# Kernel optimization log

Measured on AMD Instinct MI355X. Metric: run time of the kernel, lower is better.

Reference implementation:

```python
import jax, jax.numpy as jnp
import numpy as np

N, E, D, SD, SH, EA, FC, H = 50000, 800000, 128, 64, 16, 32, 128, 8
EPS = 1e-5


def setup_inputs() -> dict:
    key = jax.random.key(0)
    ks = jax.random.split(key, 20)
    rn = lambda k, shp, fan: jax.random.normal(k, shp, jnp.float32) / np.sqrt(fan).astype(np.float32)
    return {
        'node_features': jax.random.normal(ks[0], (N, D), jnp.float32),
        'edge_attr': jax.random.normal(ks[1], (E, EA), jnp.float32),
        'edge_sh': jax.random.normal(ks[2], (E, SH), jnp.float32),
        'W_node': rn(ks[3], (D, D), D),
        'fc1': rn(ks[4], (EA, FC), EA), 'b1': jnp.zeros((FC,), jnp.float32),
        'fc2': rn(ks[5], (FC, FC), FC), 'b2': jnp.zeros((FC,), jnp.float32),
        'fc3': rn(ks[6], (FC, D), FC), 'b3': jnp.zeros((D,), jnp.float32),
        'W_sh': rn(ks[7], (SH, D), SH),
        'aW1': rn(ks[8], (2 * SD + EA, FC), 2 * SD + EA), 'ab1': jnp.zeros((FC,), jnp.float32),
        'aW2': rn(ks[9], (FC, FC), FC), 'ab2': jnp.zeros((FC,), jnp.float32),
        'aW3': rn(ks[10], (FC, H), FC), 'ab3': jnp.zeros((H,), jnp.float32),
        'W_out': rn(ks[11], (D, D), D),
        'edge_index': jax.random.randint(ks[12], (2, E), 0, N, jnp.int32),
        'batch': jnp.zeros((N,), jnp.int32),
    }


def reference(node_features, edge_attr, edge_sh, W_node, fc1, b1, fc2, b2, fc3, b3,
              W_sh, aW1, ab1, aW2, ab2, aW3, ab3, W_out, edge_index, batch):
    src, dst = edge_index[0], edge_index[1]
    x_src = node_features[src]                          # [E, D] gather
    # SeparableFCTP message MLP: radial FC net gates a depthwise TP with edge_sh
    h = jax.nn.silu(edge_attr @ fc1 + b1)
    h = jax.nn.silu(h @ fc2 + b2)
    scale = h @ fc3 + b3                                # [E, D] per-channel radial weights
    msg = jax.nn.silu((x_src @ W_node) * scale + edge_sh @ W_sh)  # [E, D]
    # edge attention over scalar channels (softmax over the edge dim, as in source)
    alpha_in = jnp.concatenate([x_src[:, :SD], node_features[dst, :SD], edge_attr], axis=-1)
    a = jax.nn.silu(alpha_in @ aW1 + ab1)
    a = jax.nn.silu(a @ aW2 + ab2)
    a = a @ aW3 + ab3                                   # [E, H]
    alpha = jax.nn.softmax(a, axis=0)
    alpha_mean = alpha.mean(axis=1, keepdims=True)      # [E, 1]
    agg = jax.ops.segment_sum(msg * alpha_mean, dst, num_segments=node_features.shape[0])
    out = node_features + agg @ W_out                   # dropout is identity in eval
    mu = out.mean(axis=-1, keepdims=True)
    var = out.var(axis=-1, keepdims=True)
    return (out - mu) / jnp.sqrt(var + EPS)
```

## Files before the change

kernel.cpp:

```cpp
#include <hip/hip_runtime.h>
#include <math.h>

#define N_NODES 50000
#define N_EDGES 800000
#define DIM     128
#define SDIM    64
#define SH_DIM  16
#define EA_DIM  32
#define FC_DIM  128
#define H_HEADS 8
#define AIN_DIM 160
#define LN_EPS  1e-5f

typedef __attribute__((ext_vector_type(8))) short short8;
typedef __attribute__((ext_vector_type(4))) short short4v;
typedef __attribute__((ext_vector_type(4))) float f32x4;

#define FR_FC1 0
#define FR_FC2 512
#define FR_FC3 2560
#define FR_WND 4608
#define FR_WSH 6656
#define FR_AW1 7168
#define FR_AW2 9728
#define FR_AW3 11776
#define FR_TOTAL 12032

__device__ __forceinline__ float silu(float x) {
    return x * __builtin_amdgcn_rcpf(1.0f + __expf(-x));
}

__device__ __forceinline__ unsigned short f2bf(float x) {
    unsigned u = __float_as_uint(x);
    return (unsigned short)((u + 0x7FFFu + ((u >> 16) & 1u)) >> 16);
}
__device__ __forceinline__ float bf2f(unsigned short h) { return __uint_as_float(((unsigned)h) << 16); }

__device__ __forceinline__ unsigned int fmap(float f) {
    unsigned int b = __float_as_uint(f);
    return (b & 0x80000000u) ? ~b : (b | 0x80000000u);
}
__device__ __forceinline__ float funmap(unsigned int u) {
    return (u & 0x80000000u) ? __uint_as_float(u & 0x7FFFFFFFu) : __uint_as_float(~u);
}

template<int KSTEPS, int NT, int STRIDE>
__device__ __forceinline__ void mm_acc(const char* aBase, int rowBase, int lane,
                                       const short8* __restrict__ bfrag, f32x4* acc)
{
    const int row  = rowBase + (lane & 15);
    const int swz  = (row & 7) << 4;
    const int rb   = row * STRIDE;
    const int koff = (lane >> 4) << 4;
    #pragma unroll
    for (int ks = 0; ks < KSTEPS; ++ks) {
        short8 a = *(const short8*)(aBase + ((rb + ks * 64 + koff) ^ swz));
        #pragma unroll
        for (int ct = 0; ct < NT; ++ct) {
            short8 b = bfrag[(ks * NT + ct) * 64 + lane];
            acc[ct] = __builtin_amdgcn_mfma_f32_16x16x32_bf16(a, b, acc[ct], 0, 0, 0);
        }
    }
}

template<int STRIDE>
__device__ __forceinline__ void store_rows_silu(char* base, int rowBase, int lane,
                                                const f32x4* acc, const float* __restrict__ bias)
{
    const int l15  = lane & 15;
    const int col2 = l15 * 2;
    #pragma unroll
    for (int ct = 0; ct < 8; ++ct) {
        const float bv = bias[ct * 16 + l15];
        #pragma unroll
        for (int r = 0; r < 4; ++r) {
            const int row = rowBase + ((lane >> 4) * 4) + r;
            const float v = silu(acc[ct][r] + bv);
            const int off = (row * STRIDE + ct * 32 + col2) ^ ((row & 7) << 4);
            *(short*)(base + off) = (short)f2bf(v);
        }
    }
}

__device__ __forceinline__ void zero8(f32x4* a) {
    #pragma unroll
    for (int i = 0; i < 8; ++i) a[i] = (f32x4){0.f, 0.f, 0.f, 0.f};
}

__global__ void k_prep(const float* __restrict__ fc1, const float* __restrict__ fc2,
                       const float* __restrict__ fc3, const float* __restrict__ W_node,
                       const float* __restrict__ W_sh, const float* __restrict__ aW1,
                       const float* __restrict__ aW2, const float* __restrict__ aW3,
                       short8* __restrict__ frags)
{
    const int gid = blockIdx.x * 256 + threadIdx.x;
    const float* src; int Ksrc, Nsrc, Nld, NT, base;
    if (gid < 2560) {
        if (gid < 512)  { src = fc1;  Ksrc = 32;  Nsrc = 128; Nld = 128; NT = 8; base = FR_FC1; }
        else            { src = fc2;  Ksrc = 128; Nsrc = 128; Nld = 128; NT = 8; base = FR_FC2; }
    } else if (gid < 6656) {
        if (gid < 4608) { src = fc3;    Ksrc = 128; Nsrc = 128; Nld = 128; NT = 8; base = FR_FC3; }
        else            { src = W_node; Ksrc = 128; Nsrc = 128; Nld = 128; NT = 8; base = FR_WND; }
    } else if (gid < 9728) {
        if (gid < 7168) { src = W_sh; Ksrc = 16;  Nsrc = 128; Nld = 128; NT = 8; base = FR_WSH; }
        else            { src = aW1;  Ksrc = 160; Nsrc = 128; Nld = 128; NT = 8; base = FR_AW1; }
    } else {
        if (gid < 11776){ src = aW2;  Ksrc = 128; Nsrc = 128; Nld = 128; NT = 8; base = FR_AW2; }
        else            { src = aW3;  Ksrc = 128; Nsrc = 8;   Nld = 8;   NT = 1; base = FR_AW3; }
    }
    const int local = gid - base;
    const int lane = local & 63;
    const int tmp  = local >> 6;
    const int ct   = tmp % NT;
    const int ks   = tmp / NT;
    const int col  = ct * 16 + (lane & 15);
    const int k0   = ks * 32 + ((lane >> 4) << 3);
    unsigned short o[8];
    #pragma unroll
    for (int i = 0; i < 8; ++i) {
        const int k = k0 + i;
        const float v = (k < Ksrc && col < Nsrc) ? src[(size_t)k * Nld + col] : 0.f;
        o[i] = f2bf(v);
    }
    unsigned a = (unsigned)o[0] | ((unsigned)o[1] << 16);
    unsigned b = (unsigned)o[2] | ((unsigned)o[3] << 16);
    unsigned c = (unsigned)o[4] | ((unsigned)o[5] << 16);
    unsigned d = (unsigned)o[6] | ((unsigned)o[7] << 16);
    ((uint4*)frags)[gid] = make_uint4(a, b, c, d);
}

__global__ void k0_init(float* __restrict__ aggz, unsigned int* __restrict__ cmax,
                        float* __restrict__ csum)
{
    const int total = N_NODES * (DIM / 2);
    for (int i = blockIdx.x * blockDim.x + threadIdx.x; i < total;
         i += gridDim.x * blockDim.x)
        aggz[i] = 0.0f;
    if (blockIdx.x == 0 && threadIdx.x < H_HEADS) {
        cmax[threadIdx.x] = fmap(-3.0e38f);
        csum[threadIdx.x] = 0.0f;
    }
}

__global__ __launch_bounds__(256, 2) void k1_logits(
    const float* __restrict__ nodef, const float* __restrict__ eattr,
    const float* __restrict__ ab1, const float* __restrict__ ab2,
    const float* __restrict__ ab3,
    const short8* __restrict__ frags,
    const int* __restrict__ srcp, const int* __restrict__ dstp,
    float* __restrict__ a_out, unsigned int* __restrict__ cmax)
{
    __shared__ __align__(16) char sBuf[64 * 512 + 64 * 256];
    char* sAIN = sBuf;
    char* sG1  = sBuf + 64 * 512;
    char* sG2  = sBuf;
    __shared__ int sid[64], did[64];
    __shared__ float wmaxL[32];

    const int tid = threadIdx.x;
    const int e0  = blockIdx.x * 64;

    if (tid < 64)            sid[tid]      = srcp[e0 + tid];
    else if (tid < 128)      did[tid - 64] = dstp[e0 + tid - 64];
    __syncthreads();

    for (int idx = tid; idx < 64 * 40; idx += 256) {
        const int e = idx / 40, q = idx - e * 40;
        float4 v; int k;
        if (q < 16)      { v = ((const float4*)(nodef + (size_t)sid[e] * DIM))[q];      k = q * 4; }
        else if (q < 32) { v = ((const float4*)(nodef + (size_t)did[e] * DIM))[q - 16]; k = 64 + (q - 16) * 4; }
        else             { v = ((const float4*)(eattr + (size_t)(e0 + e) * EA_DIM))[q - 32]; k = 128 + (q - 32) * 4; }
        short4v h = {(short)f2bf(v.x), (short)f2bf(v.y), (short)f2bf(v.z), (short)f2bf(v.w)};
        *(short4v*)(sAIN + ((e * 512 + k * 2) ^ ((e & 7) << 4))) = h;
    }
    __syncthreads();

    const int lane = tid & 63, w = tid >> 6;
    const int rowBase = w * 16;
    f32x4 g[8];

    zero8(g);
    mm_acc<5, 8, 512>(sAIN, rowBase, lane, frags + FR_AW1, g);
    store_rows_silu<256>(sG1, rowBase, lane, g, ab1);
    __syncthreads();

    zero8(g);
    mm_acc<4, 8, 256>(sG1, rowBase, lane, frags + FR_AW2, g);
    store_rows_silu<256>(sG2, rowBase, lane, g, ab2);
    __syncthreads();

    f32x4 p = {0.f, 0.f, 0.f, 0.f};
    mm_acc<4, 1, 256>(sG2, rowBase, lane, frags + FR_AW3, &p);

    const int h = lane & 15;
    float vmax = -3.0e38f;
    if (h < H_HEADS) {
        const float ab = ab3[h];
        #pragma unroll
        for (int r = 0; r < 4; ++r) {
            const int row = rowBase + ((lane >> 4) * 4) + r;
            const float v = p[r] + ab;
            a_out[(size_t)(e0 + row) * H_HEADS + h] = v;
            vmax = fmaxf(vmax, v);
        }
    }
    vmax = fmaxf(vmax, __shfl_xor(vmax, 16));
    vmax = fmaxf(vmax, __shfl_xor(vmax, 32));
    if (lane < 8) wmaxL[w * 8 + lane] = vmax;
    __syncthreads();
    if (tid < 8) {
        const float m = fmaxf(fmaxf(wmaxL[tid], wmaxL[8 + tid]),
                              fmaxf(wmaxL[16 + tid], wmaxL[24 + tid]));
        atomicMax(&cmax[tid], fmap(m));
    }
}

__global__ void k2_expsum(const float* __restrict__ a_buf,
                          const unsigned int* __restrict__ cmax,
                          float* __restrict__ csum)
{
    __shared__ float partial[4][8];
    const int tid = threadIdx.x;
    const int h   = tid & 7;
    const float M = funmap(cmax[h]);
    float s = 0.f;
    const int total = N_EDGES * H_HEADS;
    const int stride = gridDim.x * 256;
    for (int i = blockIdx.x * 256 + tid; i < total; i += stride)
        s += __expf(a_buf[i] - M);
    s += __shfl_xor(s, 8);
    s += __shfl_xor(s, 16);
    s += __shfl_xor(s, 32);
    const int wave = tid >> 6, lane = tid & 63;
    if (lane < 8) partial[wave][lane] = s;
    __syncthreads();
    if (tid < 8) {
        float t = partial[0][tid] + partial[1][tid] + partial[2][tid] + partial[3][tid];
        atomicAdd(&csum[tid], t);
    }
}

__global__ __launch_bounds__(256, 2) void k3_message(
    const float* __restrict__ nodef, const float* __restrict__ eattr,
    const float* __restrict__ esh,
    const float* __restrict__ b1, const float* __restrict__ b2,
    const float* __restrict__ b3,
    const short8* __restrict__ frags,
    const int* __restrict__ srcp, const int* __restrict__ dstp,
    const float* __restrict__ a_buf, const unsigned int* __restrict__ cmax,
    const float* __restrict__ csum,
    unsigned short* __restrict__ aggB)
{
    __shared__ __align__(16) char sBuf[49152];
    char* sXS = sBuf;
    char* sEA = sBuf + 16384;
    char* sSH = sBuf + 24576;
    char* sH1 = sBuf + 32768;
    char* sH2 = sBuf + 16384;
    __shared__ float amL[64];
    __shared__ int sidL[64], didL[64];

    const int tid = threadIdx.x;
    const int e0  = blockIdx.x * 64;

    if (tid < 64)       sidL[tid]      = srcp[e0 + tid];
    else if (tid < 128) didL[tid - 64] = dstp[e0 + tid - 64];
    __syncthreads();

    for (int idx = tid; idx < 64 * 32; idx += 256) {
        const int e = idx >> 5, q = idx & 31;
        float4 v = ((const float4*)(nodef + (size_t)sidL[e] * DIM))[q];
        short4v h = {(short)f2bf(v.x), (short)f2bf(v.y), (short)f2bf(v.z), (short)f2bf(v.w)};
        *(short4v*)(sXS + ((e * 256 + q * 8) ^ ((e & 7) << 4))) = h;
    }
    for (int idx = tid; idx < 64 * 8; idx += 256) {
        const int e = idx >> 3, q = idx & 7;
        float4 v = ((const float4*)(eattr + (size_t)(e0 + e) * EA_DIM))[q];
        short4v h = {(short)f2bf(v.x), (short)f2bf(v.y), (short)f2bf(v.z), (short)f2bf(v.w)};
        *(short4v*)(sEA + ((e * 128 + q * 8) ^ ((e & 7) << 4))) = h;
    }
    for (int idx = tid; idx < 64 * 8; idx += 256) {
        const int e = idx >> 3, q = idx & 7;
        short4v h = {0, 0, 0, 0};
        if (q < 4) {
            float4 v = ((const float4*)(esh + (size_t)(e0 + e) * SH_DIM))[q];
            h = (short4v){(short)f2bf(v.x), (short)f2bf(v.y), (short)f2bf(v.z), (short)f2bf(v.w)};
        }
        *(short4v*)(sSH + ((e * 128 + q * 8) ^ ((e & 7) << 4))) = h;
    }
    if (tid < 64) {
        float s = 0.f;
        #pragma unroll
        for (int h = 0; h < H_HEADS; ++h)
            s += __expf(a_buf[(size_t)(e0 + tid) * H_HEADS + h] - funmap(cmax[h])) / csum[h];
        amL[tid] = s * (1.0f / H_HEADS);
    }
    __syncthreads();

    const int lane = tid & 63, w = tid >> 6;
    const int rowBase = w * 16;
    const int l15 = lane & 15;
    f32x4 sc[8], xw[8], sw[8];

    zero8(sw);
    mm_acc<1, 8, 128>(sSH, rowBase, lane, frags + FR_WSH, sw);

    zero8(sc);
    mm_acc<1, 8, 128>(sEA, rowBase, lane, frags + FR_FC1, sc);
    store_rows_silu<256>(sH1, rowBase, lane, sc, b1);
    __syncthreads();

    zero8(sc);
    mm_acc<4, 8, 256>(sH1, rowBase, lane, frags + FR_FC2, sc);
    store_rows_silu<256>(sH2, rowBase, lane, sc, b2);
    __syncthreads();

    zero8(sc);
    mm_acc<4, 8, 256>(sH2, rowBase, lane, frags + FR_FC3, sc);
    #pragma unroll
    for (int ct = 0; ct < 8; ++ct) sc[ct] += b3[ct * 16 + l15];

    zero8(xw);
    mm_acc<4, 8, 256>(sXS, rowBase, lane, frags + FR_WND, xw);

    #pragma unroll
    for (int r = 0; r < 4; ++r) {
        const int row = rowBase + ((lane >> 4) * 4) + r;
        const float am = amL[row];
        const unsigned long long abase =
            (unsigned long long)(aggB) + (unsigned long long)didL[row] * (DIM * 2);
        #pragma unroll
        for (int cp = 0; cp < 4; ++cp) {
            const float m0 = silu(xw[2*cp][r]   * sc[2*cp][r]   + sw[2*cp][r])   * am;
            const float m1 = silu(xw[2*cp+1][r] * sc[2*cp+1][r] + sw[2*cp+1][r]) * am;
            const unsigned u  = (unsigned)f2bf(m0) | ((unsigned)f2bf(m1) << 16);
            const unsigned un = __shfl_xor(u, 1);
            if (!(lane & 1)) {
                const unsigned p0 = (u & 0xFFFFu) | (un << 16);
                const unsigned p1 = (u >> 16) | (un & 0xFFFF0000u);
                const unsigned long long a0 = abase + (unsigned)((2*cp*16 + l15) * 2);
                const unsigned long long a1 = abase + (unsigned)(((2*cp+1)*16 + l15) * 2);
                asm volatile("global_atomic_pk_add_bf16 %0, %1, off" :: "v"(a0), "v"(p0) : "memory");
                asm volatile("global_atomic_pk_add_bf16 %0, %1, off" :: "v"(a1), "v"(p1) : "memory");
            }
        }
    }
}

#define K4_NB 16

__global__ __launch_bounds__(256, 2) void k4_out(
    const float* __restrict__ nodef, const unsigned short* __restrict__ aggB,
    const float* __restrict__ W_out, float* __restrict__ outp)
{
    __shared__ float aggL[K4_NB * 132];
    __shared__ float outL[K4_NB * 144];
    const int tid = threadIdx.x;
    const int n0  = blockIdx.x * K4_NB;

    for (int idx = tid; idx < K4_NB * 16; idx += 256) {
        const int nl = idx >> 4, q = idx & 15;
        uint4 v = ((const uint4*)(aggB))[(size_t)(n0 + nl) * 16 + q];
        float* dstp = aggL + nl * 132 + q * 8;
        dstp[0] = bf2f((unsigned short)(v.x & 0xFFFF)); dstp[1] = bf2f((unsigned short)(v.x >> 16));
        dstp[2] = bf2f((unsigned short)(v.y & 0xFFFF)); dstp[3] = bf2f((unsigned short)(v.y >> 16));
        dstp[4] = bf2f((unsigned short)(v.z & 0xFFFF)); dstp[5] = bf2f((unsigned short)(v.z >> 16));
        dstp[6] = bf2f((unsigned short)(v.w & 0xFFFF)); dstp[7] = bf2f((unsigned short)(v.w >> 16));
    }
    __syncthreads();

    const int f = tid & 127, ng = tid >> 7;
    float acc[8];
    #pragma unroll
    for (int j = 0; j < 8; ++j) acc[j] = nodef[(size_t)(n0 + ng * 8 + j) * DIM + f];
    #pragma unroll 4
    for (int k = 0; k < DIM; ++k) {
        const float wv = W_out[(size_t)k * DIM + f];
        #pragma unroll
        for (int j = 0; j < 8; ++j) acc[j] += aggL[(ng * 8 + j) * 132 + k] * wv;
    }
    #pragma unroll
    for (int j = 0; j < 8; ++j) outL[(ng * 8 + j) * 144 + f] = acc[j];
    __syncthreads();

    const int node = tid >> 4, l16 = tid & 15;
    float v[8];
    float s = 0.f;
    #pragma unroll
    for (int j = 0; j < 8; ++j) { v[j] = outL[node * 144 + l16 + j * 16]; s += v[j]; }
    #pragma unroll
    for (int m = 1; m < 16; m <<= 1) s += __shfl_xor(s, m);
    const float mu = s * (1.0f / DIM);
    float vs = 0.f;
    #pragma unroll
    for (int j = 0; j < 8; ++j) { const float d = v[j] - mu; vs += d * d; }
    #pragma unroll
    for (int m = 1; m < 16; m <<= 1) vs += __shfl_xor(vs, m);
    const float rstd = rsqrtf(vs * (1.0f / DIM) + LN_EPS);
    #pragma unroll
    for (int j = 0; j < 8; ++j)
        outp[(size_t)(n0 + node) * DIM + l16 + j * 16] = (v[j] - mu) * rstd;
}

extern "C" void kernel_launch(void* const* d_in, const int* in_sizes, int n_in,
                              void* d_out, int out_size, void* d_ws, size_t ws_size,
                              hipStream_t stream)
{
    const float* nodef  = (const float*)d_in[0];
    const float* eattr  = (const float*)d_in[1];
    const float* esh    = (const float*)d_in[2];
    const float* W_node = (const float*)d_in[3];
    const float* fc1    = (const float*)d_in[4];
    const float* b1     = (const float*)d_in[5];
    const float* fc2    = (const float*)d_in[6];
    const float* b2     = (const float*)d_in[7];
    const float* fc3    = (const float*)d_in[8];
    const float* b3     = (const float*)d_in[9];
    const float* W_sh   = (const float*)d_in[10];
    const float* aW1    = (const float*)d_in[11];
    const float* ab1    = (const float*)d_in[12];
    const float* aW2    = (const float*)d_in[13];
    const float* ab2    = (const float*)d_in[14];
    const float* aW3    = (const float*)d_in[15];
    const float* ab3    = (const float*)d_in[16];
    const float* W_out  = (const float*)d_in[17];
    const int*   eidx   = (const int*)d_in[18];
    const int* srcp = eidx;
    const int* dstp = eidx + N_EDGES;

    float* ws = (float*)d_ws;
    unsigned short* aggB = (unsigned short*)ws;
    unsigned int* cmax = (unsigned int*)(ws + 3200000);
    float* csum  = ws + 3200008;
    float* a_buf = ws + 3200016;
    short8* frags = (short8*)(ws + 9600016);
    float* outp = (float*)d_out;

    k_prep    <<<47, 256, 0, stream>>>(fc1, fc2, fc3, W_node, W_sh, aW1, aW2, aW3, frags);
    k0_init   <<<2048, 256, 0, stream>>>((float*)aggB, cmax, csum);
    k1_logits <<<N_EDGES / 64, 256, 0, stream>>>(nodef, eattr, ab1, ab2, ab3, frags,
                                                 srcp, dstp, a_buf, cmax);
    k2_expsum <<<1024, 256, 0, stream>>>(a_buf, cmax, csum);
    k3_message<<<N_EDGES / 64, 256, 0, stream>>>(nodef, eattr, esh, b1, b2, b3, frags,
                                                 srcp, dstp, a_buf, cmax, csum, aggB);
    k4_out    <<<N_NODES / K4_NB, 256, 0, stream>>>(nodef, aggB, W_out, outp);
}
```

Measured before the change: 945.4 us.

## Pre-convert node features to bf16, store logits in bf16, split MFMA work by columns

Adds a pre-pass that converts node features to bf16 once, so the edge kernels gather half as many bytes per row and skip the per-edge conversion. Attention logits are now stored as bf16, which halves the traffic in the logit write, the exp-sum pass and the message pass, at some cost in softmax precision. The MFMA work is repartitioned so each wave owns two output column tiles across all 64 rows instead of 16 rows across all columns. That loads each weight fragment once per wave and reuses it across four row tiles, but each A fragment is now read from LDS by every wave.

```diff
diff --git a/kernel.cpp b/kernel.cpp
--- a/kernel.cpp
+++ b/kernel.cpp
@@ -26,6 +26,7 @@
 #define FR_AW3 11776
 #define FR_TOTAL 12032
 
+
 __device__ __forceinline__ float silu(float x) {
     return x * __builtin_amdgcn_rcpf(1.0f + __expf(-x));
 }
@@ -42,6 +43,26 @@
 }
 __device__ __forceinline__ float funmap(unsigned int u) {
     return (u & 0x80000000u) ? __uint_as_float(u & 0x7FFFFFFFu) : __uint_as_float(~u);
+}
+
+template<int KSTEPS, int STRIDE>
+__device__ __forceinline__ void mm_col(const char* aBase, int lane, int ct0,
+                                       const short8* __restrict__ bfrag, f32x4 (*acc)[2])
+{
+    const int l15  = lane & 15;
+    const int koff = (lane >> 4) << 4;
+    #pragma unroll
+    for (int ks = 0; ks < KSTEPS; ++ks) {
+        const short8 b0 = bfrag[(ks * 8 + ct0) * 64 + lane];
+        const short8 b1 = bfrag[(ks * 8 + ct0 + 1) * 64 + lane];
+        #pragma unroll
+        for (int rs = 0; rs < 4; ++rs) {
+            const int row = rs * 16 + l15;
+            const short8 a = *(const short8*)(aBase + ((row * STRIDE + ks * 64 + koff) ^ ((row & 7) << 4)));
+            acc[rs][0] = __builtin_amdgcn_mfma_f32_16x16x32_bf16(a, b0, acc[rs][0], 0, 0, 0);
+            acc[rs][1] = __builtin_amdgcn_mfma_f32_16x16x32_bf16(a, b1, acc[rs][1], 0, 0, 0);
+        }
+    }
 }
 
 template<int KSTEPS, int NT, int STRIDE>
@@ -64,27 +85,32 @@
 }
 
 template<int STRIDE>
-__device__ __forceinline__ void store_rows_silu(char* base, int rowBase, int lane,
-                                                const f32x4* acc, const float* __restrict__ bias)
+__device__ __forceinline__ void store_col_silu(char* base, int lane, int ct0,
+                                               f32x4 (*acc)[2], const float* __restrict__ bias)
 {
     const int l15  = lane & 15;
-    const int col2 = l15 * 2;
-    #pragma unroll
-    for (int ct = 0; ct < 8; ++ct) {
-        const float bv = bias[ct * 16 + l15];
+    const float bv0 = bias[ct0 * 16 + l15];
+    const float bv1 = bias[ct0 * 16 + 16 + l15];
+    #pragma unroll
+    for (int rs = 0; rs < 4; ++rs) {
         #pragma unroll
         for (int r = 0; r < 4; ++r) {
-            const int row = rowBase + ((lane >> 4) * 4) + r;
-            const float v = silu(acc[ct][r] + bv);
-            const int off = (row * STRIDE + ct * 32 + col2) ^ ((row & 7) << 4);
-            *(short*)(base + off) = (short)f2bf(v);
-        }
-    }
-}
-
-__device__ __forceinline__ void zero8(f32x4* a) {
-    #pragma unroll
-    for (int i = 0; i < 8; ++i) a[i] = (f32x4){0.f, 0.f, 0.f, 0.f};
+            const int row = rs * 16 + ((lane >> 4) << 2) + r;
+            const int swz = (row & 7) << 4;
+            const float v0 = silu(acc[rs][0][r] + bv0);
+            const float v1 = silu(acc[rs][1][r] + bv1);
+            *(short*)(base + ((row * STRIDE + ct0 * 32 + l15 * 2) ^ swz))      = (short)f2bf(v0);
+            *(short*)(base + ((row * STRIDE + ct0 * 32 + 32 + l15 * 2) ^ swz)) = (short)f2bf(v1);
+        }
+    }
+}
+
+__device__ __forceinline__ void zerocol(f32x4 (*a)[2]) {
+    #pragma unroll
+    for (int i = 0; i < 4; ++i) {
+        a[i][0] = (f32x4){0.f, 0.f, 0.f, 0.f};
+        a[i][1] = (f32x4){0.f, 0.f, 0.f, 0.f};
+    }
 }
 
 __global__ void k_prep(const float* __restrict__ fc1, const float* __restrict__ fc2,
@@ -129,6 +155,14 @@
     ((uint4*)frags)[gid] = make_uint4(a, b, c, d);
 }
 
+__global__ void k_prep2(const float* __restrict__ nodef, unsigned short* __restrict__ nodefB)
+{
+    const int i = blockIdx.x * 256 + threadIdx.x;
+    float4 v = ((const float4*)nodef)[i];
+    short4v h = {(short)f2bf(v.x), (short)f2bf(v.y), (short)f2bf(v.z), (short)f2bf(v.w)};
+    ((short4v*)nodefB)[i] = h;
+}
+
 __global__ void k0_init(float* __restrict__ aggz, unsigned int* __restrict__ cmax,
                         float* __restrict__ csum)
 {
@@ -143,12 +177,12 @@
 }
 
 __global__ __launch_bounds__(256, 2) void k1_logits(
-    const float* __restrict__ nodef, const float* __restrict__ eattr,
+    const unsigned short* __restrict__ nodefB, const float* __restrict__ eattr,
     const float* __restrict__ ab1, const float* __restrict__ ab2,
     const float* __restrict__ ab3,
     const short8* __restrict__ frags,
     const int* __restrict__ srcp, const int* __restrict__ dstp,
-    float* __restrict__ a_out, unsigned int* __restrict__ cmax)
+    unsigned short* __restrict__ a_outB, unsigned int* __restrict__ cmax)
 {
     __shared__ __align__(16) char sBuf[64 * 512 + 64 * 256];
     char* sAIN = sBuf;
@@ -164,33 +198,39 @@
     else if (tid < 128)      did[tid - 64] = dstp[e0 + tid - 64];
     __syncthreads();
 
-    for (int idx = tid; idx < 64 * 40; idx += 256) {
-        const int e = idx / 40, q = idx - e * 40;
-        float4 v; int k;
-        if (q < 16)      { v = ((const float4*)(nodef + (size_t)sid[e] * DIM))[q];      k = q * 4; }
-        else if (q < 32) { v = ((const float4*)(nodef + (size_t)did[e] * DIM))[q - 16]; k = 64 + (q - 16) * 4; }
-        else             { v = ((const float4*)(eattr + (size_t)(e0 + e) * EA_DIM))[q - 32]; k = 128 + (q - 32) * 4; }
-        short4v h = {(short)f2bf(v.x), (short)f2bf(v.y), (short)f2bf(v.z), (short)f2bf(v.w)};
-        *(short4v*)(sAIN + ((e * 512 + k * 2) ^ ((e & 7) << 4))) = h;
+    for (int idx = tid; idx < 64 * 24; idx += 256) {
+        const int e = idx / 24, q = idx - e * 24;
+        if (q < 16) {
+            const int node = (q < 8) ? sid[e] : did[e];
+            const int qq = q & 7;
+            short8 v = ((const short8*)(nodefB + (size_t)node * DIM))[qq];
+            const int k = (q < 8 ? 0 : 64) + qq * 8;
+            *(short8*)(sAIN + ((e * 512 + k * 2) ^ ((e & 7) << 4))) = v;
+        } else {
+            float4 v = ((const float4*)(eattr + (size_t)(e0 + e) * EA_DIM))[q - 16];
+            short4v h = {(short)f2bf(v.x), (short)f2bf(v.y), (short)f2bf(v.z), (short)f2bf(v.w)};
+            const int k = 128 + (q - 16) * 4;
+            *(short4v*)(sAIN + ((e * 512 + k * 2) ^ ((e & 7) << 4))) = h;
+        }
     }
     __syncthreads();
 
     const int lane = tid & 63, w = tid >> 6;
-    const int rowBase = w * 16;
-    f32x4 g[8];
-
-    zero8(g);
-    mm_acc<5, 8, 512>(sAIN, rowBase, lane, frags + FR_AW1, g);
-    store_rows_silu<256>(sG1, rowBase, lane, g, ab1);
-    __syncthreads();
-
-    zero8(g);
-    mm_acc<4, 8, 256>(sG1, rowBase, lane, frags + FR_AW2, g);
-    store_rows_silu<256>(sG2, rowBase, lane, g, ab2);
+    const int ct0 = w * 2;
+    f32x4 acc[4][2];
+
+    zerocol(acc);
+    mm_col<5, 512>(sAIN, lane, ct0, frags + FR_AW1, acc);
+    store_col_silu<256>(sG1, lane, ct0, acc, ab1);
+    __syncthreads();
+
+    zerocol(acc);
+    mm_col<4, 256>(sG1, lane, ct0, frags + FR_AW2, acc);
+    store_col_silu<256>(sG2, lane, ct0, acc, ab2);
     __syncthreads();
 
     f32x4 p = {0.f, 0.f, 0.f, 0.f};
-    mm_acc<4, 1, 256>(sG2, rowBase, lane, frags + FR_AW3, &p);
+    mm_acc<4, 1, 256>(sG2, w * 16, lane, frags + FR_AW3, &p);
 
     const int h = lane & 15;
     float vmax = -3.0e38f;
@@ -198,10 +238,10 @@
         const float ab = ab3[h];
         #pragma unroll
         for (int r = 0; r < 4; ++r) {
-            const int row = rowBase + ((lane >> 4) * 4) + r;
-            const float v = p[r] + ab;
-            a_out[(size_t)(e0 + row) * H_HEADS + h] = v;
-            vmax = fmaxf(vmax, v);
+            const int row = w * 16 + ((lane >> 4) << 2) + r;
+            const unsigned short bv = f2bf(p[r] + ab);
+            a_outB[(size_t)(e0 + row) * H_HEADS + h] = bv;
+            vmax = fmaxf(vmax, bf2f(bv));
         }
     }
     vmax = fmaxf(vmax, __shfl_xor(vmax, 16));
@@ -215,24 +255,29 @@
     }
 }
 
-__global__ void k2_expsum(const float* __restrict__ a_buf,
+__global__ void k2_expsum(const unsigned* __restrict__ a_bufB,
                           const unsigned int* __restrict__ cmax,
                           float* __restrict__ csum)
 {
     __shared__ float partial[4][8];
     const int tid = threadIdx.x;
-    const int h   = tid & 7;
-    const float M = funmap(cmax[h]);
-    float s = 0.f;
-    const int total = N_EDGES * H_HEADS;
+    const int p   = tid & 3;
+    const float M0 = funmap(cmax[2 * p]);
+    const float M1 = funmap(cmax[2 * p + 1]);
+    float s0 = 0.f, s1 = 0.f;
+    const int total = N_EDGES * 4;
     const int stride = gridDim.x * 256;
-    for (int i = blockIdx.x * 256 + tid; i < total; i += stride)
-        s += __expf(a_buf[i] - M);
-    s += __shfl_xor(s, 8);
-    s += __shfl_xor(s, 16);
-    s += __shfl_xor(s, 32);
+    for (int i = blockIdx.x * 256 + tid; i < total; i += stride) {
+        const unsigned v = a_bufB[i];
+        s0 += __expf(bf2f((unsigned short)(v & 0xFFFFu)) - M0);
+        s1 += __expf(bf2f((unsigned short)(v >> 16)) - M1);
+    }
+    s0 += __shfl_xor(s0, 4);  s1 += __shfl_xor(s1, 4);
+    s0 += __shfl_xor(s0, 8);  s1 += __shfl_xor(s1, 8);
+    s0 += __shfl_xor(s0, 16); s1 += __shfl_xor(s1, 16);
+    s0 += __shfl_xor(s0, 32); s1 += __shfl_xor(s1, 32);
     const int wave = tid >> 6, lane = tid & 63;
-    if (lane < 8) partial[wave][lane] = s;
+    if (lane < 4) { partial[wave][lane * 2] = s0; partial[wave][lane * 2 + 1] = s1; }
     __syncthreads();
     if (tid < 8) {
         float t = partial[0][tid] + partial[1][tid] + partial[2][tid] + partial[3][tid];
@@ -241,13 +286,13 @@
 }
 
 __global__ __launch_bounds__(256, 2) void k3_message(
-    const float* __restrict__ nodef, const float* __restrict__ eattr,
+    const unsigned short* __restrict__ nodefB, const float* __restrict__ eattr,
     const float* __restrict__ esh,
     const float* __restrict__ b1, const float* __restrict__ b2,
     const float* __restrict__ b3,
     const short8* __restrict__ frags,
     const int* __restrict__ srcp, const int* __restrict__ dstp,
-    const float* __restrict__ a_buf, const unsigned int* __restrict__ cmax,
+    const unsigned short* __restrict__ a_bufB, const unsigned int* __restrict__ cmax,
     const float* __restrict__ csum,
     unsigned short* __restrict__ aggB)
 {
@@ -267,11 +312,10 @@
     else if (tid < 128) didL[tid - 64] = dstp[e0 + tid - 64];
     __syncthreads();
 
-    for (int idx = tid; idx < 64 * 32; idx += 256) {
-        const int e = idx >> 5, q = idx & 31;
-        float4 v = ((const float4*)(nodef + (size_t)sidL[e] * DIM))[q];
-        short4v h = {(short)f2bf(v.x), (short)f2bf(v.y), (short)f2bf(v.z), (short)f2bf(v.w)};
-        *(short4v*)(sXS + ((e * 256 + q * 8) ^ ((e & 7) << 4))) = h;
+    for (int idx = tid; idx < 64 * 16; idx += 256) {
+        const int e = idx >> 4, q = idx & 15;
+        short8 v = ((const short8*)(nodefB + (size_t)sidL[e] * DIM))[q];
+        *(short8*)(sXS + ((e * 256 + q * 16) ^ ((e & 7) << 4))) = v;
     }
     for (int idx = tid; idx < 64 * 8; idx += 256) {
         const int e = idx >> 3, q = idx & 7;
@@ -289,57 +333,57 @@
         *(short4v*)(sSH + ((e * 128 + q * 8) ^ ((e & 7) << 4))) = h;
     }
     if (tid < 64) {
+        uint4 v = ((const uint4*)a_bufB)[e0 + tid];
+        const unsigned short* pv = (const unsigned short*)&v;
         float s = 0.f;
         #pragma unroll
         for (int h = 0; h < H_HEADS; ++h)
-            s += __expf(a_buf[(size_t)(e0 + tid) * H_HEADS + h] - funmap(cmax[h])) / csum[h];
+            s += __expf(bf2f(pv[h]) - funmap(cmax[h])) * __builtin_amdgcn_rcpf(csum[h]);
         amL[tid] = s * (1.0f / H_HEADS);
     }
     __syncthreads();
 
     const int lane = tid & 63, w = tid >> 6;
-    const int rowBase = w * 16;
-    const int l15 = lane & 15;
-    f32x4 sc[8], xw[8], sw[8];
-
-    zero8(sw);
-    mm_acc<1, 8, 128>(sSH, rowBase, lane, frags + FR_WSH, sw);
-
-    zero8(sc);
-    mm_acc<1, 8, 128>(sEA, rowBase, lane, frags + FR_FC1, sc);
-    store_rows_silu<256>(sH1, rowBase, lane, sc, b1);
-    __syncthreads();
-
-    zero8(sc);
-    mm_acc<4, 8, 256>(sH1, rowBase, lane, frags + FR_FC2, sc);
-    store_rows_silu<256>(sH2, rowBase, lane, sc, b2);
-    __syncthreads();
-
-    zero8(sc);
-    mm_acc<4, 8, 256>(sH2, rowBase, lane, frags + FR_FC3, sc);
-    #pragma unroll
-    for (int ct = 0; ct < 8; ++ct) sc[ct] += b3[ct * 16 + l15];
-
-    zero8(xw);
-    mm_acc<4, 8, 256>(sXS, rowBase, lane, frags + FR_WND, xw);
-
-    #pragma unroll
-    for (int r = 0; r < 4; ++r) {
-        const int row = rowBase + ((lane >> 4) * 4) + r;
-        const float am = amL[row];
-        const unsigned long long abase =
-            (unsigned long long)(aggB) + (unsigned long long)didL[row] * (DIM * 2);
-        #pragma unroll
-        for (int cp = 0; cp < 4; ++cp) {
-            const float m0 = silu(xw[2*cp][r]   * sc[2*cp][r]   + sw[2*cp][r])   * am;
-            const float m1 = silu(xw[2*cp+1][r] * sc[2*cp+1][r] + sw[2*cp+1][r]) * am;
+    const int ct0 = w * 2, l15 = lane & 15;
+    f32x4 sw[4][2], sc[4][2], xw[4][2];
+
+    zerocol(sw);
+    mm_col<1, 128>(sSH, lane, ct0, frags + FR_WSH, sw);
+    zerocol(sc);
+    mm_col<1, 128>(sEA, lane, ct0, frags + FR_FC1, sc);
+    store_col_silu<256>(sH1, lane, ct0, sc, b1);
+    __syncthreads();
+
+    zerocol(sc);
+    mm_col<4, 256>(sH1, lane, ct0, frags + FR_FC2, sc);
+    store_col_silu<256>(sH2, lane, ct0, sc, b2);
+    __syncthreads();
+
+    zerocol(sc);
+    mm_col<4, 256>(sH2, lane, ct0, frags + FR_FC3, sc);
+    zerocol(xw);
+    mm_col<4, 256>(sXS, lane, ct0, frags + FR_WND, xw);
+
+    const float bv0 = b3[ct0 * 16 + l15];
+    const float bv1 = b3[ct0 * 16 + 16 + l15];
+
+    #pragma unroll
+    for (int rs = 0; rs < 4; ++rs) {
+        #pragma unroll
+        for (int r = 0; r < 4; ++r) {
+            const int row = rs * 16 + ((lane >> 4) << 2) + r;
+            const float am = amL[row];
+            const float m0 = silu(xw[rs][0][r] * (sc[rs][0][r] + bv0) + sw[rs][0][r]) * am;
+            const float m1 = silu(xw[rs][1][r] * (sc[rs][1][r] + bv1) + sw[rs][1][r]) * am;
             const unsigned u  = (unsigned)f2bf(m0) | ((unsigned)f2bf(m1) << 16);
             const unsigned un = __shfl_xor(u, 1);
             if (!(lane & 1)) {
                 const unsigned p0 = (u & 0xFFFFu) | (un << 16);
                 const unsigned p1 = (u >> 16) | (un & 0xFFFF0000u);
-                const unsigned long long a0 = abase + (unsigned)((2*cp*16 + l15) * 2);
-                const unsigned long long a1 = abase + (unsigned)(((2*cp+1)*16 + l15) * 2);
+                const unsigned long long abase =
+                    (unsigned long long)aggB + (unsigned long long)didL[row] * (DIM * 2);
+                const unsigned long long a0 = abase + (unsigned)((ct0 * 16 + l15) * 2);
+                const unsigned long long a1 = abase + (unsigned)((ct0 * 16 + 16 + l15) * 2);
                 asm volatile("global_atomic_pk_add_bf16 %0, %1, off" :: "v"(a0), "v"(p0) : "memory");
                 asm volatile("global_atomic_pk_add_bf16 %0, %1, off" :: "v"(a1), "v"(p1) : "memory");
             }
@@ -429,19 +473,21 @@
     const int* dstp = eidx + N_EDGES;
 
     float* ws = (float*)d_ws;
-    unsigned short* aggB = (unsigned short*)ws;
-    unsigned int* cmax = (unsigned int*)(ws + 3200000);
-    float* csum  = ws + 3200008;
-    float* a_buf = ws + 3200016;
-    short8* frags = (short8*)(ws + 9600016);
+    unsigned short* aggB  = (unsigned short*)ws;
+    unsigned int*   cmax  = (unsigned int*)(ws + 3200000);
+    float*          csum  = ws + 3200008;
+    unsigned short* a_bufB = (unsigned short*)(ws + 3200016);
+    short8*         frags = (short8*)(ws + 6400016);
+    unsigned short* nodefB = (unsigned short*)(ws + 6448144);
     float* outp = (float*)d_out;
 
     k_prep    <<<47, 256, 0, stream>>>(fc1, fc2, fc3, W_node, W_sh, aW1, aW2, aW3, frags);
+    k_prep2   <<<N_NODES * DIM / 4 / 256, 256, 0, stream>>>(nodef, nodefB);
     k0_init   <<<2048, 256, 0, stream>>>((float*)aggB, cmax, csum);
-    k1_logits <<<N_EDGES / 64, 256, 0, stream>>>(nodef, eattr, ab1, ab2, ab3, frags,
-                                                 srcp, dstp, a_buf, cmax);
-    k2_expsum <<<1024, 256, 0, stream>>>(a_buf, cmax, csum);
-    k3_message<<<N_EDGES / 64, 256, 0, stream>>>(nodef, eattr, esh, b1, b2, b3, frags,
-                                                 srcp, dstp, a_buf, cmax, csum, aggB);
+    k1_logits <<<N_EDGES / 64, 256, 0, stream>>>(nodefB, eattr, ab1, ab2, ab3, frags,
+                                                 srcp, dstp, a_bufB, cmax);
+    k2_expsum <<<1024, 256, 0, stream>>>((const unsigned*)a_bufB, cmax, csum);
+    k3_message<<<N_EDGES / 64, 256, 0, stream>>>(nodefB, eattr, esh, b1, b2, b3, frags,
+                                                 srcp, dstp, a_bufB, cmax, csum, aggB);
     k4_out    <<<N_NODES / K4_NB, 256, 0, stream>>>(nodef, aggB, W_out, outp);
 }
```

Measured after the change: 868.5 us. 8.1% less time.
